# Optimization experiments

Hardware: AMD Instinct MI355X
Metric: run time of the kernel (lower is better)

The kernel has to match this reference:

```python
import jax, jax.numpy as jnp
import numpy as np

B, N, C = 1, 512, 128  # batch, seq (pair rows/cols), pair channel dim
EPS = 1e-5
ENDING = False  # 'outgoing' triangle update (ending=False in the torch module)


def layer_norm(x, w, b):
    mu = jnp.mean(x, axis=-1, keepdims=True)
    var = jnp.mean(jnp.square(x - mu), axis=-1, keepdims=True)
    return (x - mu) * jax.lax.rsqrt(var + EPS) * w + b


def setup_inputs() -> dict:
    key = jax.random.key(0)
    ks = jax.random.split(key, 10)
    s = 0.02
    return {
        "x": jax.random.normal(ks[0], (B, N, N, C), dtype=jnp.float32),
        "norm_in_w": jnp.ones((C,), jnp.float32),
        "norm_in_b": jnp.zeros((C,), jnp.float32),
        "g_in_w": jax.random.normal(ks[1], (2 * C, C), jnp.float32) * s,
        "p_in_w": jax.random.normal(ks[2], (2 * C, C), jnp.float32) * s,
        "g_out_w": jax.random.normal(ks[3], (C, C), jnp.float32) * s,
        "norm_out_w": jnp.ones((C,), jnp.float32),
        "norm_out_b": jnp.zeros((C,), jnp.float32),
        "p_out_w": jax.random.normal(ks[4], (C, C), jnp.float32) * s,
    }


def reference(x, norm_in_w, norm_in_b, g_in_w, p_in_w, g_out_w,
              norm_out_w, norm_out_b, p_out_w):
    # LN -> fused g/p/g_out projections (no bias, as in Boltz)
    xn = layer_norm(x, norm_in_w, norm_in_b)                      # [B,N,N,C]
    g_in = jax.nn.sigmoid(jnp.einsum('bijc,dc->bijd', xn, g_in_w))  # [B,N,N,2C]
    p_in = jnp.einsum('bijc,dc->bijd', xn, p_in_w)                  # [B,N,N,2C]
    pg = p_in * g_in                                                # gated projections
    a = pg[..., :C]   # left projection  [B,N,N,C]
    b = pg[..., C:]   # right projection [B,N,N,C]
    if ENDING:
        tri = jnp.einsum('bkic,bkjc->bijc', a, b)  # incoming edges
    else:
        tri = jnp.einsum('bikc,bjkc->bijc', a, b)  # outgoing edges
    out = layer_norm(tri, norm_out_w, norm_out_b)
    out = jnp.einsum('bijc,dc->bijd', out, p_out_w)                 # [B,N,N,C]
    gate = jax.nn.sigmoid(jnp.einsum('bijc,dc->bijd', xn, g_out_w))
    return out * gate
```

## Files before the change

kernel.cpp:

```cpp
#include <hip/hip_runtime.h>

typedef __bf16 bf16;
typedef __bf16 bf16x4 __attribute__((ext_vector_type(4)));
typedef __bf16 bf16x8 __attribute__((ext_vector_type(8)));
typedef float floatx4 __attribute__((ext_vector_type(4)));

#define NN 512
#define CC 128
#define NROW (NN*NN)

__device__ __forceinline__ void async16(void* lds, const void* g) {
    __builtin_amdgcn_global_load_lds((const __attribute__((address_space(1))) void*)g,
                                     (__attribute__((address_space(3))) void*)lds, 16, 0, 0);
}
__device__ __forceinline__ void wait_vm0() {
    asm volatile("s_waitcnt vmcnt(0)" ::: "memory");
}
__device__ __forceinline__ float sigmoidf(float x) {
    return __builtin_amdgcn_rcpf(1.f + __expf(-x));
}

__global__ void setup_kernel(const float* __restrict__ nin_w, const float* __restrict__ nin_b,
                             const float* __restrict__ g_in_w, const float* __restrict__ p_in_w,
                             const float* __restrict__ g_out_w,
                             const float* __restrict__ nout_w, const float* __restrict__ nout_b,
                             const float* __restrict__ p_out_w,
                             bf16* __restrict__ Wall, float* __restrict__ T1, float* __restrict__ T2,
                             bf16* __restrict__ Pp, float* __restrict__ S1, float* __restrict__ S2) {
    int r = blockIdx.x * 256 + threadIdx.x;
    if (r < 640) {
        const float* src = (r < 256) ? (g_in_w + r*CC)
                         : (r < 512) ? (p_in_w + (r-256)*CC)
                                     : (g_out_w + (r-512)*CC);
        float t1 = 0.f, t2 = 0.f;
        for (int c = 0; c < CC; ++c) {
            float wv = src[c];
            float wn = nin_w[c];
            float bn = nin_b[c];
            Wall[r*CC + c] = (bf16)(wv * wn);
            t1 += wn * wv;
            t2 += bn * wv;
        }
        T1[r] = t1; T2[r] = t2;
    } else if (r < 768) {
        int d = r - 640;
        const float* src = p_out_w + d*CC;
        float t1 = 0.f, t2 = 0.f;
        for (int c = 0; c < CC; ++c) {
            float wv = src[c];
            float wn = nout_w[c];
            float bn = nout_b[c];
            Pp[d*CC + c] = (bf16)(wv * wn);
            t1 += wn * wv;
            t2 += bn * wv;
        }
        S1[d] = t1; S2[d] = t2;
    }
}

__global__ __launch_bounds__(256) void k1_ln_proj(
        const float* __restrict__ x, const bf16* __restrict__ Wall,
        const float* __restrict__ T1, const float* __restrict__ T2,
        bf16* __restrict__ a_t, bf16* __restrict__ b_t, bf16* __restrict__ gate) {
    __shared__ char  XNb[16384];
    __shared__ float MU[64], RS[64];

    const int t    = threadIdx.x;
    const int w    = t >> 6, lane = t & 63;
    const int col  = lane & 15, quad = lane >> 4;
    const long r0  = (long)blockIdx.x * 64;

    const int row  = t >> 2;
    const int part = t & 3;
    const float* xr = x + (r0 + row) * CC;
    floatx4 f[8];
#pragma unroll
    for (int j = 0; j < 8; ++j)
        f[j] = *(const floatx4*)(xr + (j*4 + part)*4);

    {
        float sum = 0.f, ss = 0.f;
#pragma unroll
        for (int j = 0; j < 8; ++j)
#pragma unroll
            for (int e = 0; e < 4; ++e) { float v = f[j][e]; sum += v; ss += v*v; }
        sum += __shfl_xor(sum, 1, 64); ss += __shfl_xor(ss, 1, 64);
        sum += __shfl_xor(sum, 2, 64); ss += __shfl_xor(ss, 2, 64);
        float mu  = sum * (1.f/128.f);
        float var = ss  * (1.f/128.f) - mu*mu;
        float rs  = rsqrtf(var + 1e-5f);
        if (part == 0) { MU[row] = mu; RS[row] = rs; }
    }

#pragma unroll
    for (int j = 0; j < 8; ++j) {
        int c4   = j*4 + part;
        int c16  = c4 >> 1, half = c4 & 1;
        bf16x4 v;
        v[0] = (bf16)f[j][0]; v[1] = (bf16)f[j][1];
        v[2] = (bf16)f[j][2]; v[3] = (bf16)f[j][3];
        *(bf16x4*)(XNb + row*256 + ((c16 ^ (row & 15)) * 16) + half*8) = v;
    }
    __syncthreads();

    bf16x8 af[4][4];
#pragma unroll
    for (int mt = 0; mt < 4; ++mt) {
        int rr = mt*16 + col;
#pragma unroll
        for (int s = 0; s < 4; ++s)
            af[mt][s] = *(const bf16x8*)(XNb + rr*256 + (((s*4 + quad) ^ (rr & 15)) * 16));
    }
    __syncthreads();
    char* TBw = XNb + w*3072;

    for (int jj = 0; jj < 6; ++jj) {
        int job = w + jj*4;
        if (job < 16) {
            bf16x8 bg[4], bp[4];
            for (int s = 0; s < 4; ++s) {
                bg[s] = *(const bf16x8*)(Wall + (      job*16 + col)*CC + s*32 + quad*8);
                bp[s] = *(const bf16x8*)(Wall + (256 + job*16 + col)*CC + s*32 + quad*8);
            }
            int dg = job*16 + col, dp = 256 + job*16 + col;
            float t1g = T1[dg], t2g = T2[dg], t1p = T1[dp], t2p = T2[dp];
            bf16* dst = (job < 8) ? a_t : b_t;
            int cbase = (job < 8 ? job : job - 8) * 16;
            for (int mt = 0; mt < 4; ++mt) {
                floatx4 ag = {0.f,0.f,0.f,0.f}, ap = {0.f,0.f,0.f,0.f};
            #pragma unroll
                for (int s = 0; s < 4; ++s) {
                    ag = __builtin_amdgcn_mfma_f32_16x16x32_bf16(af[mt][s], bg[s], ag, 0, 0, 0);
                    ap = __builtin_amdgcn_mfma_f32_16x16x32_bf16(af[mt][s], bp[s], ap, 0, 0, 0);
                }
                bf16x4 pk;
            #pragma unroll
                for (int reg = 0; reg < 4; ++reg) {
                    int m = mt*16 + quad*4 + reg;
                    float rs = RS[m], mu = MU[m];
                    float g = rs*ag[reg] - rs*mu*t1g + t2g;
                    float p = rs*ap[reg] - rs*mu*t1p + t2p;
                    pk[reg] = (bf16)(p * sigmoidf(g));
                }
                *(bf16x4*)(TBw + col*144 + mt*32 + quad*8) = pk;
            }
            {
                int c  = lane >> 2;
                int c0 = lane & 3, c1 = (lane & 3) + 4;
                bf16x8 r0v = *(const bf16x8*)(TBw + c*144 + c0*16);
                bf16x8 r1v = *(const bf16x8*)(TBw + c*144 + c1*16);
                bf16* base = dst + (long)(cbase + c) * NROW + r0;
                *(bf16x8*)(base + c0*8) = r0v;
                *(bf16x8*)(base + c1*8) = r1v;
            }
        } else {
            int gc = job - 16;
            bf16x8 bgt[4];
            for (int s = 0; s < 4; ++s)
                bgt[s] = *(const bf16x8*)(Wall + (512 + gc*16 + col)*CC + s*32 + quad*8);
            int dd = 512 + gc*16 + col;
            float t1 = T1[dd], t2 = T2[dd];
            for (int mt = 0; mt < 4; ++mt) {
                floatx4 ac = {0.f,0.f,0.f,0.f};
            #pragma unroll
                for (int s = 0; s < 4; ++s)
                    ac = __builtin_amdgcn_mfma_f32_16x16x32_bf16(af[mt][s], bgt[s], ac, 0, 0, 0);
            #pragma unroll
                for (int reg = 0; reg < 4; ++reg) {
                    int m = mt*16 + quad*4 + reg;
                    float rs = RS[m], mu = MU[m];
                    float g = rs*ac[reg] - rs*mu*t1 + t2;
                    *(bf16*)(TBw + m*48 + col*2) = (bf16)sigmoidf(g);
                }
            }
            {
                bf16x8 g0 = *(const bf16x8*)(TBw + lane*48 + 0);
                bf16x8 g1 = *(const bf16x8*)(TBw + lane*48 + 16);
                bf16* gdst = gate + (r0 + lane)*CC + gc*16;
                *(bf16x8*)(gdst + 0) = g0;
                *(bf16x8*)(gdst + 8) = g1;
            }
        }
    }
}

__global__ __launch_bounds__(256, 2) void k2_tri(
        const bf16* __restrict__ a_t, const bf16* __restrict__ b_t, bf16* __restrict__ tri) {
    __shared__ char As[16384], Bs[8192];
    const int t    = threadIdx.x;
    const int w    = t >> 6, lane = t & 63;
    const int col  = lane & 15, quad = lane >> 4;
    const int c    = blockIdx.y;
    const int i0   = (blockIdx.x >> 2) * 256, j0 = (blockIdx.x & 3) * 128;
    const char* Ac = (const char*)(a_t + (long)c * NROW);
    const char* Bc = (const char*)(b_t + (long)c * NROW);
    const int wm = w * 64;

    floatx4 acc[4][8];
    for (int mt = 0; mt < 4; ++mt)
        for (int nt = 0; nt < 8; ++nt) { floatx4 z = {0.f,0.f,0.f,0.f}; acc[mt][nt] = z; }

    for (int k0 = 0; k0 < 512; k0 += 32) {
        __syncthreads();
        for (int q = 0; q < 4; ++q) {
            int L = q*4096 + t*16;
            int row = L >> 6, p = (L >> 4) & 3;
            int cl = p ^ ((row >> 2) & 3);
            async16(As + L, Ac + (i0 + row)*1024 + k0*2 + cl*16);
        }
        for (int q = 0; q < 2; ++q) {
            int L = q*4096 + t*16;
            int row = L >> 6, p = (L >> 4) & 3;
            int cl = p ^ ((row >> 2) & 3);
            async16(Bs + L, Bc + (j0 + row)*1024 + k0*2 + cl*16);
        }
        wait_vm0();
        __syncthreads();
        bf16x8 afr[4], bfr[8];
        for (int mt = 0; mt < 4; ++mt) {
            int row = wm + mt*16 + col;
            afr[mt] = *(const bf16x8*)(As + row*64 + ((quad ^ ((row>>2)&3))*16));
        }
        for (int nt = 0; nt < 8; ++nt) {
            int row = nt*16 + col;
            bfr[nt] = *(const bf16x8*)(Bs + row*64 + ((quad ^ ((row>>2)&3))*16));
        }
        for (int mt = 0; mt < 4; ++mt)
            for (int nt = 0; nt < 8; ++nt)
                acc[mt][nt] = __builtin_amdgcn_mfma_f32_16x16x32_bf16(afr[mt], bfr[nt], acc[mt][nt], 0, 0, 0);
    }
    bf16* Tc = tri + (long)c * NROW;
    for (int mt = 0; mt < 4; ++mt)
        for (int nt = 0; nt < 8; ++nt)
            for (int reg = 0; reg < 4; ++reg) {
                int m = i0 + wm + mt*16 + quad*4 + reg;
                int n = j0 + nt*16 + col;
                Tc[m*512 + n] = (bf16)acc[mt][nt][reg];
            }
}

__global__ __launch_bounds__(256) void k3_out(
        const bf16* __restrict__ tri, const bf16* __restrict__ Pp,
        const float* __restrict__ S1, const float* __restrict__ S2,
        const bf16* __restrict__ gate, float* __restrict__ out) {
    __shared__ char  AS[128*272];
    __shared__ float MU[128], RS[128];
    const int t    = threadIdx.x;
    const int w    = t >> 6, lane = t & 63;
    const int col  = lane & 15, quad = lane >> 4;
    const long r0  = (long)blockIdx.x * 128;

    for (int it = 0; it < 16; ++it) {
        int rl = (it & 1)*64 + (t & 63);
        int cq = (it >> 1)*4 + (t >> 6);
        const bf16* src = tri + (long)(cq*4) * NROW + r0 + rl;
        bf16x4 v;
        v[0] = src[0];
        v[1] = src[NROW];
        v[2] = src[2*NROW];
        v[3] = src[3*NROW];
        *(bf16x4*)(AS + rl*272 + cq*8) = v;
    }
    __syncthreads();

    {
        int row = t >> 1, half = t & 1;
        float sum = 0.f, ss = 0.f;
        for (int j = 0; j < 8; ++j) {
            bf16x8 v = *(const bf16x8*)(AS + row*272 + (half*8 + j)*16);
            for (int jj = 0; jj < 8; ++jj) { float f = (float)v[jj]; sum += f; ss += f*f; }
        }
        sum += __shfl_xor(sum, 1, 64);
        ss  += __shfl_xor(ss, 1, 64);
        float mu  = sum * (1.f/128.f);
        float var = ss  * (1.f/128.f) - mu*mu;
        float rs  = rsqrtf(var + 1e-5f);
        if (half == 0) { MU[row] = mu; RS[row] = rs; }
    }
    __syncthreads();

    const int wm = (w >> 1)*64, wn = (w & 1)*64;
    floatx4 acc[4][4];
    for (int mt = 0; mt < 4; ++mt)
        for (int nt = 0; nt < 4; ++nt) { floatx4 z = {0.f,0.f,0.f,0.f}; acc[mt][nt] = z; }

    for (int s = 0; s < 4; ++s) {
        bf16x8 bfr[4];
        for (int nt = 0; nt < 4; ++nt)
            bfr[nt] = *(const bf16x8*)(Pp + (wn + nt*16 + col)*CC + s*32 + quad*8);
        for (int mt = 0; mt < 4; ++mt) {
            int row = wm + mt*16 + col;
            bf16x8 afr = *(const bf16x8*)(AS + row*272 + s*64 + quad*16);
            for (int nt = 0; nt < 4; ++nt)
                acc[mt][nt] = __builtin_amdgcn_mfma_f32_16x16x32_bf16(afr, bfr[nt], acc[mt][nt], 0, 0, 0);
        }
    }

    for (int mt = 0; mt < 4; ++mt)
        for (int nt = 0; nt < 4; ++nt) {
            int n = wn + nt*16 + col;
            float s1 = S1[n], s2 = S2[n];
            for (int reg = 0; reg < 4; ++reg) {
                int m = wm + mt*16 + quad*4 + reg;
                float rs = RS[m], mu = MU[m];
                float v  = rs*acc[mt][nt][reg] - rs*mu*s1 + s2;
                float gt = (float)gate[(r0 + m)*CC + n];
                out[(r0 + m)*CC + n] = v * gt;
            }
        }
}

extern "C" void kernel_launch(void* const* d_in, const int* in_sizes, int n_in,
                              void* d_out, int out_size, void* d_ws, size_t ws_size,
                              hipStream_t stream) {
    const float* x       = (const float*)d_in[0];
    const float* nin_w   = (const float*)d_in[1];
    const float* nin_b   = (const float*)d_in[2];
    const float* g_in_w  = (const float*)d_in[3];
    const float* p_in_w  = (const float*)d_in[4];
    const float* g_out_w = (const float*)d_in[5];
    const float* nout_w  = (const float*)d_in[6];
    const float* nout_b  = (const float*)d_in[7];
    const float* p_out_w = (const float*)d_in[8];

    char* ws = (char*)d_ws;
    bf16*  Wall = (bf16*)(ws);
    float* T1   = (float*)(ws + 163840);
    float* T2   = (float*)(ws + 166400);
    bf16*  Pp   = (bf16*)(ws + 168960);
    float* S1   = (float*)(ws + 201728);
    float* S2   = (float*)(ws + 202240);
    const long BIG = 67108864L;
    bf16* a_t  = (bf16*)(ws + 204800);
    bf16* b_t  = (bf16*)(ws + 204800 + BIG);
    bf16* gate = (bf16*)(ws + 204800 + 2*BIG);
    bf16* tri  = (bf16*)(ws + 204800 + 3*BIG);
    float* outp = (float*)d_out;

    setup_kernel<<<3, 256, 0, stream>>>(nin_w, nin_b, g_in_w, p_in_w, g_out_w,
                                        nout_w, nout_b, p_out_w,
                                        Wall, T1, T2, Pp, S1, S2);
    k1_ln_proj<<<4096, 256, 0, stream>>>(x, Wall, T1, T2, a_t, b_t, gate);
    k2_tri<<<dim3(8, 128), 256, 0, stream>>>(a_t, b_t, tri);
    k3_out<<<2048, 256, 0, stream>>>(tri, Pp, S1, S2, gate, outp);
}
```

Before: 537.3 us.

## Double-buffer tri GEMM, remap blocks, vectorize k3 transpose, cut k1 register pressure

k2_tri now double-buffers its A/B LDS tiles so the async global-to-LDS load of the next k-step overlaps the current MFMAs. Its 1D grid is remapped so that consecutive workgroups work on different channels. k3_out replaces scalar strided bf16 gathers from tri with 16-byte vector loads, transposed into LDS through an XOR-swizzled slot layout to cut bank conflicts. k1 moves the staging buffer to its own LDS array and reloads A fragments per m-tile instead of holding all 16 in registers, trading extra LDS reads for lower register pressure.

```diff
diff --git a/kernel.cpp b/kernel.cpp
--- a/kernel.cpp
+++ b/kernel.cpp
@@ -63,6 +63,7 @@
         const float* __restrict__ T1, const float* __restrict__ T2,
         bf16* __restrict__ a_t, bf16* __restrict__ b_t, bf16* __restrict__ gate) {
     __shared__ char  XNb[16384];
+    __shared__ char  TB[12288];
     __shared__ float MU[64], RS[64];
 
     const int t    = threadIdx.x;
@@ -103,16 +104,7 @@
     }
     __syncthreads();
 
-    bf16x8 af[4][4];
-#pragma unroll
-    for (int mt = 0; mt < 4; ++mt) {
-        int rr = mt*16 + col;
-#pragma unroll
-        for (int s = 0; s < 4; ++s)
-            af[mt][s] = *(const bf16x8*)(XNb + rr*256 + (((s*4 + quad) ^ (rr & 15)) * 16));
-    }
-    __syncthreads();
-    char* TBw = XNb + w*3072;
+    char* TBw = TB + w*3072;
 
     for (int jj = 0; jj < 6; ++jj) {
         int job = w + jj*4;
@@ -127,11 +119,16 @@
             bf16* dst = (job < 8) ? a_t : b_t;
             int cbase = (job < 8 ? job : job - 8) * 16;
             for (int mt = 0; mt < 4; ++mt) {
+                int rr = mt*16 + col;
+                bf16x8 afm[4];
+            #pragma unroll
+                for (int s = 0; s < 4; ++s)
+                    afm[s] = *(const bf16x8*)(XNb + rr*256 + (((s*4 + quad) ^ (rr & 15)) * 16));
                 floatx4 ag = {0.f,0.f,0.f,0.f}, ap = {0.f,0.f,0.f,0.f};
             #pragma unroll
                 for (int s = 0; s < 4; ++s) {
-                    ag = __builtin_amdgcn_mfma_f32_16x16x32_bf16(af[mt][s], bg[s], ag, 0, 0, 0);
-                    ap = __builtin_amdgcn_mfma_f32_16x16x32_bf16(af[mt][s], bp[s], ap, 0, 0, 0);
+                    ag = __builtin_amdgcn_mfma_f32_16x16x32_bf16(afm[s], bg[s], ag, 0, 0, 0);
+                    ap = __builtin_amdgcn_mfma_f32_16x16x32_bf16(afm[s], bp[s], ap, 0, 0, 0);
                 }
                 bf16x4 pk;
             #pragma unroll
@@ -161,10 +158,15 @@
             int dd = 512 + gc*16 + col;
             float t1 = T1[dd], t2 = T2[dd];
             for (int mt = 0; mt < 4; ++mt) {
+                int rr = mt*16 + col;
+                bf16x8 afm[4];
+            #pragma unroll
+                for (int s = 0; s < 4; ++s)
+                    afm[s] = *(const bf16x8*)(XNb + rr*256 + (((s*4 + quad) ^ (rr & 15)) * 16));
                 floatx4 ac = {0.f,0.f,0.f,0.f};
             #pragma unroll
                 for (int s = 0; s < 4; ++s)
-                    ac = __builtin_amdgcn_mfma_f32_16x16x32_bf16(af[mt][s], bgt[s], ac, 0, 0, 0);
+                    ac = __builtin_amdgcn_mfma_f32_16x16x32_bf16(afm[s], bgt[s], ac, 0, 0, 0);
             #pragma unroll
                 for (int reg = 0; reg < 4; ++reg) {
                     int m = mt*16 + quad*4 + reg;
@@ -184,14 +186,32 @@
     }
 }
 
+__device__ __forceinline__ void k2_stage(char* Asb, char* Bsb, const char* Ac, const char* Bc,
+                                         int i0, int j0, int k0, int t) {
+    for (int q = 0; q < 4; ++q) {
+        int L = q*4096 + t*16;
+        int row = L >> 6, p = (L >> 4) & 3;
+        int cl = p ^ ((row >> 2) & 3);
+        async16(Asb + L, Ac + (i0 + row)*1024 + k0*2 + cl*16);
+    }
+    for (int q = 0; q < 2; ++q) {
+        int L = q*4096 + t*16;
+        int row = L >> 6, p = (L >> 4) & 3;
+        int cl = p ^ ((row >> 2) & 3);
+        async16(Bsb + L, Bc + (j0 + row)*1024 + k0*2 + cl*16);
+    }
+}
+
 __global__ __launch_bounds__(256, 2) void k2_tri(
         const bf16* __restrict__ a_t, const bf16* __restrict__ b_t, bf16* __restrict__ tri) {
-    __shared__ char As[16384], Bs[8192];
+    __shared__ char As[2][16384], Bs[2][8192];
     const int t    = threadIdx.x;
     const int w    = t >> 6, lane = t & 63;
     const int col  = lane & 15, quad = lane >> 4;
-    const int c    = blockIdx.y;
-    const int i0   = (blockIdx.x >> 2) * 256, j0 = (blockIdx.x & 3) * 128;
+    const int wg   = blockIdx.x;
+    const int c    = (wg & 7) + ((wg >> 6) << 3);
+    const int tile = (wg >> 3) & 7;
+    const int i0   = (tile >> 2) * 256, j0 = (tile & 3) * 128;
     const char* Ac = (const char*)(a_t + (long)c * NROW);
     const char* Bc = (const char*)(b_t + (long)c * NROW);
     const int wm = w * 64;
@@ -200,34 +220,29 @@
     for (int mt = 0; mt < 4; ++mt)
         for (int nt = 0; nt < 8; ++nt) { floatx4 z = {0.f,0.f,0.f,0.f}; acc[mt][nt] = z; }
 
-    for (int k0 = 0; k0 < 512; k0 += 32) {
-        __syncthreads();
-        for (int q = 0; q < 4; ++q) {
-            int L = q*4096 + t*16;
-            int row = L >> 6, p = (L >> 4) & 3;
-            int cl = p ^ ((row >> 2) & 3);
-            async16(As + L, Ac + (i0 + row)*1024 + k0*2 + cl*16);
-        }
-        for (int q = 0; q < 2; ++q) {
-            int L = q*4096 + t*16;
-            int row = L >> 6, p = (L >> 4) & 3;
-            int cl = p ^ ((row >> 2) & 3);
-            async16(Bs + L, Bc + (j0 + row)*1024 + k0*2 + cl*16);
-        }
-        wait_vm0();
-        __syncthreads();
+    k2_stage(As[0], Bs[0], Ac, Bc, i0, j0, 0, t);
+    wait_vm0();
+    __syncthreads();
+
+    int cur = 0;
+    for (int kt = 0; kt < 16; ++kt) {
+        if (kt < 15)
+            k2_stage(As[cur^1], Bs[cur^1], Ac, Bc, i0, j0, (kt+1)*32, t);
         bf16x8 afr[4], bfr[8];
         for (int mt = 0; mt < 4; ++mt) {
             int row = wm + mt*16 + col;
-            afr[mt] = *(const bf16x8*)(As + row*64 + ((quad ^ ((row>>2)&3))*16));
+            afr[mt] = *(const bf16x8*)(As[cur] + row*64 + ((quad ^ ((row>>2)&3))*16));
         }
         for (int nt = 0; nt < 8; ++nt) {
             int row = nt*16 + col;
-            bfr[nt] = *(const bf16x8*)(Bs + row*64 + ((quad ^ ((row>>2)&3))*16));
+            bfr[nt] = *(const bf16x8*)(Bs[cur] + row*64 + ((quad ^ ((row>>2)&3))*16));
         }
         for (int mt = 0; mt < 4; ++mt)
             for (int nt = 0; nt < 8; ++nt)
                 acc[mt][nt] = __builtin_amdgcn_mfma_f32_16x16x32_bf16(afr[mt], bfr[nt], acc[mt][nt], 0, 0, 0);
+        wait_vm0();
+        __syncthreads();
+        cur ^= 1;
     }
     bf16* Tc = tri + (long)c * NROW;
     for (int mt = 0; mt < 4; ++mt)
@@ -250,16 +265,22 @@
     const int col  = lane & 15, quad = lane >> 4;
     const long r0  = (long)blockIdx.x * 128;
 
-    for (int it = 0; it < 16; ++it) {
-        int rl = (it & 1)*64 + (t & 63);
-        int cq = (it >> 1)*4 + (t >> 6);
-        const bf16* src = tri + (long)(cq*4) * NROW + r0 + rl;
-        bf16x4 v;
-        v[0] = src[0];
-        v[1] = src[NROW];
-        v[2] = src[2*NROW];
-        v[3] = src[3*NROW];
-        *(bf16x4*)(AS + rl*272 + cq*8) = v;
+    for (int it = 0; it < 2; ++it) {
+        int grp = it*16 + (t >> 4);
+        int c0  = grp*4;
+        int jb  = (t & 15)*8;
+        const bf16* src = tri + (long)c0 * NROW + r0 + jb;
+        bf16x8 p0 = *(const bf16x8*)(src);
+        bf16x8 p1 = *(const bf16x8*)(src + NROW);
+        bf16x8 p2 = *(const bf16x8*)(src + 2*NROW);
+        bf16x8 p3 = *(const bf16x8*)(src + 3*NROW);
+        int slot = grp ^ ((t & 3) << 1);
+    #pragma unroll
+        for (int j = 0; j < 8; ++j) {
+            bf16x4 v;
+            v[0] = p0[j]; v[1] = p1[j]; v[2] = p2[j]; v[3] = p3[j];
+            *(bf16x4*)(AS + (jb + j)*272 + slot*8) = v;
+        }
     }
     __syncthreads();
 
@@ -267,7 +288,8 @@
         int row = t >> 1, half = t & 1;
         float sum = 0.f, ss = 0.f;
         for (int j = 0; j < 8; ++j) {
-            bf16x8 v = *(const bf16x8*)(AS + row*272 + (half*8 + j)*16);
+            int ch = (half*8 + j) ^ ((row >> 3) & 3);
+            bf16x8 v = *(const bf16x8*)(AS + row*272 + ch*16);
             for (int jj = 0; jj < 8; ++jj) { float f = (float)v[jj]; sum += f; ss += f*f; }
         }
         sum += __shfl_xor(sum, 1, 64);
@@ -290,7 +312,8 @@
             bfr[nt] = *(const bf16x8*)(Pp + (wn + nt*16 + col)*CC + s*32 + quad*8);
         for (int mt = 0; mt < 4; ++mt) {
             int row = wm + mt*16 + col;
-            bf16x8 afr = *(const bf16x8*)(AS + row*272 + s*64 + quad*16);
+            int ch  = (s*4 + quad) ^ ((row >> 3) & 3);
+            bf16x8 afr = *(const bf16x8*)(AS + row*272 + ch*16);
             for (int nt = 0; nt < 4; ++nt)
                 acc[mt][nt] = __builtin_amdgcn_mfma_f32_16x16x32_bf16(afr, bfr[nt], acc[mt][nt], 0, 0, 0);
         }
@@ -341,6 +364,6 @@
                                         nout_w, nout_b, p_out_w,
                                         Wall, T1, T2, Pp, S1, S2);
     k1_ln_proj<<<4096, 256, 0, stream>>>(x, Wall, T1, T2, a_t, b_t, gate);
-    k2_tri<<<dim3(8, 128), 256, 0, stream>>>(a_t, b_t, tri);
+    k2_tri<<<1024, 256, 0, stream>>>(a_t, b_t, tri);
     k3_out<<<2048, 256, 0, stream>>>(tri, Pp, S1, S2, gate, outp);
 }
```

Result: faster. 515.4 us (-4.1%).
